# Performance work log

Measured on AMD Instinct MI355X. Metric: run time of the kernel, lower is better.

The kernel has to match this reference:

```python
import jax, jax.numpy as jnp
import numpy as np

N_NODES = 10000
N_EDGES = 640000
DIM = 128


def setup_inputs() -> dict:
    key = jax.random.key(0)
    ks = jax.random.split(key, 10)
    s = 1.0 / np.sqrt(DIM)
    return {
        "x": jax.random.normal(ks[0], (N_NODES, DIM), dtype=jnp.float32),
        "edge_index": jax.random.randint(ks[1], (2, N_EDGES), 0, N_NODES, dtype=jnp.int64),
        "fc_w": jax.random.normal(ks[2], (DIM, DIM), dtype=jnp.float32) * s,
        "fc_b": jax.random.normal(ks[3], (DIM,), dtype=jnp.float32) * s,
        "f_lw": jax.random.normal(ks[4], (DIM, DIM), dtype=jnp.float32) * s,
        "f_lb": jax.random.normal(ks[5], (DIM,), dtype=jnp.float32) * s,
        "f_rw": jax.random.normal(ks[6], (DIM, DIM), dtype=jnp.float32) * s,
        "n_lw": jax.random.normal(ks[7], (DIM, DIM), dtype=jnp.float32) * s,
        "n_lb": jax.random.normal(ks[8], (DIM,), dtype=jnp.float32) * s,
        "n_rw": jax.random.normal(ks[9], (DIM, DIM), dtype=jnp.float32) * s,
    }


def _sage_conv(h, src, dst, lw, lb, rw, n_nodes):
    # mean aggregation of source-node features at target nodes
    msg = h[src]                                                   # [E, D]
    summed = jax.ops.segment_sum(msg, dst, num_segments=n_nodes)   # [N, D]
    cnt = jax.ops.segment_sum(jnp.ones_like(dst, dtype=h.dtype), dst, num_segments=n_nodes)
    agg = summed / jnp.maximum(cnt, 1.0)[:, None]
    # PyG SAGEConv: lin_l(agg) + lin_r(x); lin_l has bias, lin_r does not
    return agg @ lw.T + lb + h @ rw.T


def reference(x, edge_index, fc_w, fc_b, f_lw, f_lb, f_rw, n_lw, n_lb, n_rw):
    n_nodes = x.shape[0]
    src, dst = edge_index[0], edge_index[1]
    inp = x @ fc_w.T + fc_b                                        # fc residual branch
    h = jax.nn.relu(_sage_conv(x, src, dst, f_lw, f_lb, f_rw, n_nodes))
    # dropout(p=0.3) is identity in eval mode
    h = _sage_conv(h, src, dst, n_lw, n_lb, n_rw, n_nodes)
    return jax.nn.relu(h + inp)
```

## Files before the change

### kernel.cpp

```cpp
#include <hip/hip_runtime.h>
#include <hip/hip_fp8.h>

#define NN 10000
#define NE 640000
#define DIM 128
#define NB2 625
#define RC2 1280
#define EPB 4096
#define G_FILL 157
#define MT1 157
#define NODECAP 128

typedef __attribute__((ext_vector_type(8))) short bf16x8;
typedef __attribute__((ext_vector_type(4))) float f32x4;

__device__ __forceinline__ unsigned short f2bf(float f) {
    unsigned u = __float_as_uint(f);
    u += 0x7FFFu + ((u >> 16) & 1u);
    return (unsigned short)(u >> 16);
}
__device__ __forceinline__ unsigned char f2f8(float f) {
    __hip_fp8_e4m3 t(f);
    return (unsigned char)t.__x;
}
__device__ __forceinline__ float f82f(unsigned char u) {
    __hip_fp8_e4m3 t;
    t.__x = (__hip_fp8_storage_t)u;
    return (float)t;
}
__device__ __forceinline__ bf16x8 cvt8(const float* p) {
    float4 v0 = *(const float4*)p;
    float4 v1 = *(const float4*)(p + 4);
    bf16x8 f;
    f[0] = (short)f2bf(v0.x); f[1] = (short)f2bf(v0.y);
    f[2] = (short)f2bf(v0.z); f[3] = (short)f2bf(v0.w);
    f[4] = (short)f2bf(v1.x); f[5] = (short)f2bf(v1.y);
    f[6] = (short)f2bf(v1.z); f[7] = (short)f2bf(v1.w);
    return f;
}

__device__ __forceinline__ void gather8(const unsigned char* __restrict__ g8,
                                        const unsigned short* lst,
                                        int deg, int d8, float* a) {
#pragma unroll
    for (int j = 0; j < 8; ++j) a[j] = 0.f;
    union U { uint2 v; unsigned char c[8]; };
    int r = 0;
    for (; r + 8 <= deg; r += 8) {
        U u[8];
#pragma unroll
        for (int t = 0; t < 8; ++t)
            u[t].v = *(const uint2*)(const void*)(g8 + (size_t)lst[r + t] * DIM + d8 * 8);
#pragma unroll
        for (int t = 0; t < 8; ++t)
#pragma unroll
            for (int j = 0; j < 8; ++j) a[j] += f82f(u[t].c[j]);
    }
    for (; r < deg; ++r) {
        U u0;
        u0.v = *(const uint2*)(const void*)(g8 + (size_t)lst[r] * DIM + d8 * 8);
#pragma unroll
        for (int j = 0; j < 8; ++j) a[j] += f82f(u0.c[j]);
    }
}

__global__ __launch_bounds__(256) void k1_k(
        const float* __restrict__ x,
        const int* __restrict__ src, const int* __restrict__ dst,
        const float* __restrict__ f_lw, const float* __restrict__ f_rw,
        const float* __restrict__ fc_w,
        unsigned char* __restrict__ xl8, float* __restrict__ xr, float* __restrict__ xc,
        int* __restrict__ gcur, unsigned* __restrict__ region) {
    __shared__ int start[NB2 + 1];
    __shared__ int cur[NB2];
    __shared__ int gbase[NB2];
    __shared__ int tsum[256];
    __shared__ unsigned sorted[EPB];
    const int b = blockIdx.x;
    const int tid = threadIdx.x;
    if (b < G_FILL) {
        for (int i = tid; i < NB2 + 1; i += 256) start[i] = 0;
        __syncthreads();
        int base = b * EPB;
        int nE = min(EPB, NE - base);
        unsigned pk[4][4];
        int kb[4][4];
        bool cv[4];
#pragma unroll
        for (int c = 0; c < 4; ++c) {
            int e = base + c * 1024 + tid * 4;
            cv[c] = (e < NE);
            if (cv[c]) {
                int4 s4 = *(const int4*)(src + e);
                int4 d4 = *(const int4*)(dst + e);
                pk[c][0] = ((unsigned)d4.x << 16) | (unsigned)s4.x;
                pk[c][1] = ((unsigned)d4.y << 16) | (unsigned)s4.y;
                pk[c][2] = ((unsigned)d4.z << 16) | (unsigned)s4.z;
                pk[c][3] = ((unsigned)d4.w << 16) | (unsigned)s4.w;
                kb[c][0] = d4.x >> 4; kb[c][1] = d4.y >> 4;
                kb[c][2] = d4.z >> 4; kb[c][3] = d4.w >> 4;
            }
        }
#pragma unroll
        for (int c = 0; c < 4; ++c)
            if (cv[c])
#pragma unroll
                for (int j = 0; j < 4; ++j) atomicAdd(&start[kb[c][j] + 1], 1);
        __syncthreads();
        {
            int s = 0;
            int i0 = 1 + tid * 3;
#pragma unroll
            for (int k = 0; k < 3; ++k) {
                int idx = i0 + k;
                if (idx < NB2 + 1) s += start[idx];
            }
            tsum[tid] = s;
            __syncthreads();
            for (int off = 1; off < 256; off <<= 1) {
                int v = 0;
                if (tid >= off) v = tsum[tid - off];
                __syncthreads();
                tsum[tid] += v;
                __syncthreads();
            }
            int run = (tid == 0) ? 0 : tsum[tid - 1];
#pragma unroll
            for (int k = 0; k < 3; ++k) {
                int idx = i0 + k;
                if (idx < NB2 + 1) { run += start[idx]; start[idx] = run; }
            }
        }
        __syncthreads();
        for (int i = tid; i < NB2; i += 256) cur[i] = start[i];
        __syncthreads();
#pragma unroll
        for (int c = 0; c < 4; ++c)
            if (cv[c])
#pragma unroll
                for (int j = 0; j < 4; ++j) {
                    int q = atomicAdd(&cur[kb[c][j]], 1);
                    sorted[q] = pk[c][j];
                }
        __syncthreads();
        for (int i = tid; i < NB2; i += 256) {
            int len = start[i + 1] - start[i];
            gbase[i] = (len > 0) ? atomicAdd(&gcur[i], len) : 0;
        }
        __syncthreads();
        for (int i = tid; i < nE; i += 256) {
            unsigned e = sorted[i];
            int bb = (int)(e >> 16) >> 4;
            int rel = gbase[bb] + (i - start[bb]);
            if (rel < RC2) region[(size_t)bb * RC2 + rel] = e;
        }
        return;
    }
    int jj = b - G_FILL;
    int plane = jj / MT1;
    int mt = jj - plane * MT1;
    const float* W = (plane == 0) ? f_lw : (plane == 1) ? f_rw : fc_w;
    int lane = tid & 63, wv = tid >> 6;
    int mr = lane & 15, q = lane >> 4;
    int m0 = mt * 64 + wv * 16;
    int mc = min(m0 + mr, NN - 1);
    bf16x8 afr[4];
#pragma unroll
    for (int kc = 0; kc < 4; ++kc)
        afr[kc] = cvt8(x + (size_t)mc * DIM + kc * 32 + q * 8);
    f32x4 acc[8];
#pragma unroll
    for (int nt = 0; nt < 8; ++nt) acc[nt] = (f32x4){0.f, 0.f, 0.f, 0.f};
#pragma unroll
    for (int nt = 0; nt < 8; ++nt) {
        const float* wp = W + (size_t)(nt * 16 + mr) * DIM;
#pragma unroll
        for (int kc = 0; kc < 4; ++kc) {
            bf16x8 wfr = cvt8(wp + kc * 32 + q * 8);
            acc[nt] = __builtin_amdgcn_mfma_f32_16x16x32_bf16(afr[kc], wfr, acc[nt], 0, 0, 0);
        }
    }
#pragma unroll
    for (int r = 0; r < 4; ++r) {
        int ms = m0 + q * 4 + r;
        if (ms >= NN) continue;
        if (plane == 0) {
#pragma unroll
            for (int nt = 0; nt < 8; ++nt)
                xl8[(size_t)ms * DIM + nt * 16 + mr] = f2f8(acc[nt][r]);
        } else {
            float* o = (plane == 1) ? xr : xc;
#pragma unroll
            for (int nt = 0; nt < 8; ++nt)
                o[(size_t)ms * DIM + nt * 16 + mr] = acc[nt][r];
        }
    }
}

__global__ __launch_bounds__(256) void k2_k(
        const unsigned char* __restrict__ xl8, const float* __restrict__ xr,
        const float* __restrict__ f_lb,
        const int* __restrict__ gcur, const unsigned* __restrict__ region,
        unsigned short* __restrict__ h1b, unsigned char* __restrict__ h18,
        unsigned short* __restrict__ glist, int* __restrict__ gcnt) {
    __shared__ int cnt[16];
    __shared__ unsigned short list[16][NODECAP];
    const int b = blockIdx.x;
    const int tid = threadIdx.x;
    if (tid < 16) cnt[tid] = 0;
    __syncthreads();
    const int n0 = b * 16;
    const int R = min(gcur[b], RC2);
    const unsigned* reg = region + (size_t)b * RC2;
    for (int i = tid; i < R; i += 256) {
        unsigned e = reg[i];
        int nl = (int)(e >> 16) - n0;
        if ((unsigned)nl < 16u) {
            int slot = atomicAdd(&cnt[nl], 1);
            if (slot < NODECAP) list[nl][slot] = (unsigned short)(e & 0xFFFFu);
        }
    }
    __syncthreads();
    {
        const int4* ls = (const int4*)&list[0][0];
        int4* gd = (int4*)(void*)(glist + (size_t)b * (16 * NODECAP));
        gd[tid] = ls[tid];
        if (tid < 16) gcnt[n0 + tid] = cnt[tid];
    }
    const int g = tid >> 4, d8 = tid & 15;
    const int node = n0 + g;
    const int trueDeg = cnt[g];
    const int deg = min(trueDeg, NODECAP);
    float a[8];
    gather8(xl8, &list[g][0], deg, d8, a);
    float inv = 1.f / fmaxf((float)trueDeg, 1.f);
    const float* xp = xr + (size_t)node * DIM + d8 * 8;
    float4 r0 = *(const float4*)xp;
    float4 r1 = *(const float4*)(xp + 4);
    const float* bp = f_lb + d8 * 8;
    float4 c0 = *(const float4*)bp;
    float4 c1 = *(const float4*)(bp + 4);
    float rv[8] = {r0.x, r0.y, r0.z, r0.w, r1.x, r1.y, r1.z, r1.w};
    float bv[8] = {c0.x, c0.y, c0.z, c0.w, c1.x, c1.y, c1.z, c1.w};
    union B { int4 v; unsigned short us[8]; } o;
    union U8 { uint2 v; unsigned char c[8]; } o8;
#pragma unroll
    for (int j = 0; j < 8; ++j) {
        float v = fmaxf(a[j] * inv + rv[j] + bv[j], 0.f);
        o.us[j] = f2bf(v);
        o8.c[j] = f2f8(v);
    }
    *(int4*)(void*)(h1b + (size_t)node * DIM + d8 * 8) = o.v;
    *(uint2*)(void*)(h18 + (size_t)node * DIM + d8 * 8) = o8.v;
}

__global__ __launch_bounds__(256) void k3_k(
        const unsigned char* __restrict__ h18, const unsigned short* __restrict__ h1b,
        const float* __restrict__ n_lw, const float* __restrict__ n_rw,
        const float* __restrict__ n_lb, const float* __restrict__ fc_b,
        const float* __restrict__ xc,
        const unsigned short* __restrict__ glist, const int* __restrict__ gcnt,
        float* __restrict__ out) {
    __shared__ int cnt[16];
    __shared__ unsigned short list[16][NODECAP];
    __shared__ unsigned short m1t[16][DIM];
    const int b = blockIdx.x;
    const int tid = threadIdx.x;
    {
        int4* ls = (int4*)&list[0][0];
        const int4* gs = (const int4*)(const void*)(glist + (size_t)b * (16 * NODECAP));
        ls[tid] = gs[tid];
        if (tid < 16) cnt[tid] = gcnt[b * 16 + tid];
    }
    __syncthreads();
    const int g = tid >> 4, d8 = tid & 15;
    const int trueDeg = cnt[g];
    const int deg = min(trueDeg, NODECAP);
    float a[8];
    gather8(h18, &list[g][0], deg, d8, a);
    float inv = 1.f / fmaxf((float)trueDeg, 1.f);
    union B { int4 v; unsigned short us[8]; } mo;
#pragma unroll
    for (int j = 0; j < 8; ++j) mo.us[j] = f2bf(a[j] * inv);
    *(int4*)(void*)(&m1t[g][d8 * 8]) = mo.v;
    __syncthreads();
    const int lane = tid & 63, wv = tid >> 6;
    const int mr = lane & 15, q = lane >> 4;
    const int m0 = b * 16;
    bf16x8 a0[4], a1[4];
#pragma unroll
    for (int kc = 0; kc < 4; ++kc) {
        a0[kc] = *(const bf16x8*)(const void*)(&m1t[mr][kc * 32 + q * 8]);
        a1[kc] = *(const bf16x8*)(const void*)(h1b + (size_t)(m0 + mr) * DIM + kc * 32 + q * 8);
    }
    f32x4 acc[2];
    acc[0] = (f32x4){0.f, 0.f, 0.f, 0.f};
    acc[1] = (f32x4){0.f, 0.f, 0.f, 0.f};
#pragma unroll
    for (int ntl = 0; ntl < 2; ++ntl) {
        int nt = wv * 2 + ntl;
        const float* w0p = n_lw + (size_t)(nt * 16 + mr) * DIM;
        const float* w1p = n_rw + (size_t)(nt * 16 + mr) * DIM;
#pragma unroll
        for (int kc = 0; kc < 4; ++kc) {
            bf16x8 wf0 = cvt8(w0p + kc * 32 + q * 8);
            acc[ntl] = __builtin_amdgcn_mfma_f32_16x16x32_bf16(a0[kc], wf0, acc[ntl], 0, 0, 0);
            bf16x8 wf1 = cvt8(w1p + kc * 32 + q * 8);
            acc[ntl] = __builtin_amdgcn_mfma_f32_16x16x32_bf16(a1[kc], wf1, acc[ntl], 0, 0, 0);
        }
    }
#pragma unroll
    for (int ntl = 0; ntl < 2; ++ntl) {
        int col = (wv * 2 + ntl) * 16 + mr;
        float bias = n_lb[col] + fc_b[col];
#pragma unroll
        for (int r = 0; r < 4; ++r) {
            int ms = m0 + q * 4 + r;
            float v = acc[ntl][r] + xc[(size_t)ms * DIM + col] + bias;
            out[(size_t)ms * DIM + col] = fmaxf(v, 0.f);
        }
    }
}

extern "C" void kernel_launch(void* const* d_in, const int* in_sizes, int n_in,
                              void* d_out, int out_size, void* d_ws, size_t ws_size,
                              hipStream_t stream) {
    const float* x    = (const float*)d_in[0];
    const int*   edge = (const int*)d_in[1];
    const float* fc_w = (const float*)d_in[2];
    const float* fc_b = (const float*)d_in[3];
    const float* f_lw = (const float*)d_in[4];
    const float* f_lb = (const float*)d_in[5];
    const float* f_rw = (const float*)d_in[6];
    const float* n_lw = (const float*)d_in[7];
    const float* n_lb = (const float*)d_in[8];
    const float* n_rw = (const float*)d_in[9];
    float* out = (float*)d_out;

    const int* src = edge;
    const int* dst = edge + NE;

    char* p = (char*)d_ws;
    float* xr = (float*)p;                    p += (size_t)NN * DIM * sizeof(float);
    float* xc = (float*)p;                    p += (size_t)NN * DIM * sizeof(float);
    unsigned short* h1b = (unsigned short*)p; p += (size_t)NN * DIM * sizeof(unsigned short);
    unsigned char* xl8 = (unsigned char*)p;   p += (size_t)NN * DIM;
    unsigned char* h18 = (unsigned char*)p;   p += (size_t)NN * DIM;
    unsigned short* glist = (unsigned short*)p; p += (size_t)NB2 * 16 * NODECAP * sizeof(unsigned short);
    int* gcnt = (int*)p;                      p += (size_t)NN * sizeof(int);
    int* gcur = (int*)p;                      p += 4096;
    unsigned* region = (unsigned*)p;

    hipMemsetAsync(gcur, 0, NB2 * sizeof(int), stream);
    k1_k<<<G_FILL + 3 * MT1, 256, 0, stream>>>(
        x, src, dst, f_lw, f_rw, fc_w, xl8, xr, xc, gcur, region);
    k2_k<<<NB2, 256, 0, stream>>>(xl8, xr, f_lb, gcur, region, h1b, h18, glist, gcnt);
    k3_k<<<NB2, 256, 0, stream>>>(h18, h1b, n_lw, n_rw, n_lb, fc_b, xc, glist, gcnt, out);
}
```

Before: 143.3 us.

## Fuse three kernels into one persistent kernel with grid barriers

Merges the bucket-fill/GEMM, first SAGE aggregation and second aggregation+GEMM kernels into a single launch of 628 blocks separated by software grid barriers on global atomics. Each block keeps its per-node edge list and its bf16 h1 tile in shared memory across phases, which removes the glist/gcnt/h1b global round-trips and two kernel launch gaps. It relies on all 628 blocks being co-resident (launch_bounds 256,3 on 256 CUs). If they are not, the spin barriers deadlock, and the barriers add spin/sleep latency.

```diff
diff --git a/kernel.cpp b/kernel.cpp
--- a/kernel.cpp
+++ b/kernel.cpp
@@ -10,6 +10,7 @@
 #define G_FILL 157
 #define MT1 157
 #define NODECAP 128
+#define GRID 628
 
 typedef __attribute__((ext_vector_type(8))) short bf16x8;
 typedef __attribute__((ext_vector_type(4))) float f32x4;
@@ -64,21 +65,39 @@
     }
 }
 
-__global__ __launch_bounds__(256) void k1_k(
+__device__ __forceinline__ void gridbar(int* bar) {
+    __syncthreads();
+    if (threadIdx.x == 0) {
+        __threadfence();
+        __hip_atomic_fetch_add(bar, 1, __ATOMIC_RELEASE, __HIP_MEMORY_SCOPE_AGENT);
+        while (__hip_atomic_load(bar, __ATOMIC_ACQUIRE, __HIP_MEMORY_SCOPE_AGENT) < GRID)
+            __builtin_amdgcn_s_sleep(8);
+        __threadfence();
+    }
+    __syncthreads();
+}
+
+__global__ __launch_bounds__(256, 3) void fused_k(
         const float* __restrict__ x,
         const int* __restrict__ src, const int* __restrict__ dst,
-        const float* __restrict__ f_lw, const float* __restrict__ f_rw,
-        const float* __restrict__ fc_w,
+        const float* __restrict__ f_lw, const float* __restrict__ f_lb,
+        const float* __restrict__ f_rw, const float* __restrict__ fc_w,
+        const float* __restrict__ fc_b, const float* __restrict__ n_lw,
+        const float* __restrict__ n_lb, const float* __restrict__ n_rw,
         unsigned char* __restrict__ xl8, float* __restrict__ xr, float* __restrict__ xc,
-        int* __restrict__ gcur, unsigned* __restrict__ region) {
-    __shared__ int start[NB2 + 1];
-    __shared__ int cur[NB2];
-    __shared__ int gbase[NB2];
-    __shared__ int tsum[256];
-    __shared__ unsigned sorted[EPB];
+        unsigned char* __restrict__ h18,
+        int* __restrict__ gcur, unsigned* __restrict__ region,
+        int* __restrict__ bar, float* __restrict__ out) {
+    __shared__ int sh[6228];
     const int b = blockIdx.x;
     const int tid = threadIdx.x;
+
     if (b < G_FILL) {
+        int* start = sh;
+        int* cur   = sh + 626;
+        int* gbase = sh + 1251;
+        int* tsum  = sh + 1876;
+        unsigned* sorted = (unsigned*)(sh + 2132);
         for (int i = tid; i < NB2 + 1; i += 256) start[i] = 0;
         __syncthreads();
         int base = b * EPB;
@@ -154,170 +173,144 @@
             int rel = gbase[bb] + (i - start[bb]);
             if (rel < RC2) region[(size_t)bb * RC2 + rel] = e;
         }
-        return;
-    }
-    int jj = b - G_FILL;
-    int plane = jj / MT1;
-    int mt = jj - plane * MT1;
-    const float* W = (plane == 0) ? f_lw : (plane == 1) ? f_rw : fc_w;
-    int lane = tid & 63, wv = tid >> 6;
-    int mr = lane & 15, q = lane >> 4;
-    int m0 = mt * 64 + wv * 16;
-    int mc = min(m0 + mr, NN - 1);
-    bf16x8 afr[4];
-#pragma unroll
-    for (int kc = 0; kc < 4; ++kc)
-        afr[kc] = cvt8(x + (size_t)mc * DIM + kc * 32 + q * 8);
-    f32x4 acc[8];
-#pragma unroll
-    for (int nt = 0; nt < 8; ++nt) acc[nt] = (f32x4){0.f, 0.f, 0.f, 0.f};
-#pragma unroll
-    for (int nt = 0; nt < 8; ++nt) {
-        const float* wp = W + (size_t)(nt * 16 + mr) * DIM;
-#pragma unroll
-        for (int kc = 0; kc < 4; ++kc) {
-            bf16x8 wfr = cvt8(wp + kc * 32 + q * 8);
-            acc[nt] = __builtin_amdgcn_mfma_f32_16x16x32_bf16(afr[kc], wfr, acc[nt], 0, 0, 0);
-        }
-    }
-#pragma unroll
-    for (int r = 0; r < 4; ++r) {
-        int ms = m0 + q * 4 + r;
-        if (ms >= NN) continue;
-        if (plane == 0) {
-#pragma unroll
-            for (int nt = 0; nt < 8; ++nt)
-                xl8[(size_t)ms * DIM + nt * 16 + mr] = f2f8(acc[nt][r]);
-        } else {
-            float* o = (plane == 1) ? xr : xc;
-#pragma unroll
-            for (int nt = 0; nt < 8; ++nt)
-                o[(size_t)ms * DIM + nt * 16 + mr] = acc[nt][r];
-        }
-    }
-}
-
-__global__ __launch_bounds__(256) void k2_k(
-        const unsigned char* __restrict__ xl8, const float* __restrict__ xr,
-        const float* __restrict__ f_lb,
-        const int* __restrict__ gcur, const unsigned* __restrict__ region,
-        unsigned short* __restrict__ h1b, unsigned char* __restrict__ h18,
-        unsigned short* __restrict__ glist, int* __restrict__ gcnt) {
-    __shared__ int cnt[16];
-    __shared__ unsigned short list[16][NODECAP];
-    const int b = blockIdx.x;
-    const int tid = threadIdx.x;
-    if (tid < 16) cnt[tid] = 0;
-    __syncthreads();
-    const int n0 = b * 16;
-    const int R = min(gcur[b], RC2);
-    const unsigned* reg = region + (size_t)b * RC2;
-    for (int i = tid; i < R; i += 256) {
-        unsigned e = reg[i];
-        int nl = (int)(e >> 16) - n0;
-        if ((unsigned)nl < 16u) {
-            int slot = atomicAdd(&cnt[nl], 1);
-            if (slot < NODECAP) list[nl][slot] = (unsigned short)(e & 0xFFFFu);
-        }
-    }
-    __syncthreads();
-    {
-        const int4* ls = (const int4*)&list[0][0];
-        int4* gd = (int4*)(void*)(glist + (size_t)b * (16 * NODECAP));
-        gd[tid] = ls[tid];
-        if (tid < 16) gcnt[n0 + tid] = cnt[tid];
-    }
-    const int g = tid >> 4, d8 = tid & 15;
-    const int node = n0 + g;
-    const int trueDeg = cnt[g];
-    const int deg = min(trueDeg, NODECAP);
-    float a[8];
-    gather8(xl8, &list[g][0], deg, d8, a);
-    float inv = 1.f / fmaxf((float)trueDeg, 1.f);
-    const float* xp = xr + (size_t)node * DIM + d8 * 8;
-    float4 r0 = *(const float4*)xp;
-    float4 r1 = *(const float4*)(xp + 4);
-    const float* bp = f_lb + d8 * 8;
-    float4 c0 = *(const float4*)bp;
-    float4 c1 = *(const float4*)(bp + 4);
-    float rv[8] = {r0.x, r0.y, r0.z, r0.w, r1.x, r1.y, r1.z, r1.w};
-    float bv[8] = {c0.x, c0.y, c0.z, c0.w, c1.x, c1.y, c1.z, c1.w};
-    union B { int4 v; unsigned short us[8]; } o;
-    union U8 { uint2 v; unsigned char c[8]; } o8;
-#pragma unroll
-    for (int j = 0; j < 8; ++j) {
-        float v = fmaxf(a[j] * inv + rv[j] + bv[j], 0.f);
-        o.us[j] = f2bf(v);
-        o8.c[j] = f2f8(v);
-    }
-    *(int4*)(void*)(h1b + (size_t)node * DIM + d8 * 8) = o.v;
-    *(uint2*)(void*)(h18 + (size_t)node * DIM + d8 * 8) = o8.v;
-}
-
-__global__ __launch_bounds__(256) void k3_k(
-        const unsigned char* __restrict__ h18, const unsigned short* __restrict__ h1b,
-        const float* __restrict__ n_lw, const float* __restrict__ n_rw,
-        const float* __restrict__ n_lb, const float* __restrict__ fc_b,
-        const float* __restrict__ xc,
-        const unsigned short* __restrict__ glist, const int* __restrict__ gcnt,
-        float* __restrict__ out) {
-    __shared__ int cnt[16];
-    __shared__ unsigned short list[16][NODECAP];
-    __shared__ unsigned short m1t[16][DIM];
-    const int b = blockIdx.x;
-    const int tid = threadIdx.x;
-    {
-        int4* ls = (int4*)&list[0][0];
-        const int4* gs = (const int4*)(const void*)(glist + (size_t)b * (16 * NODECAP));
-        ls[tid] = gs[tid];
-        if (tid < 16) cnt[tid] = gcnt[b * 16 + tid];
-    }
-    __syncthreads();
-    const int g = tid >> 4, d8 = tid & 15;
-    const int trueDeg = cnt[g];
-    const int deg = min(trueDeg, NODECAP);
-    float a[8];
-    gather8(h18, &list[g][0], deg, d8, a);
-    float inv = 1.f / fmaxf((float)trueDeg, 1.f);
-    union B { int4 v; unsigned short us[8]; } mo;
-#pragma unroll
-    for (int j = 0; j < 8; ++j) mo.us[j] = f2bf(a[j] * inv);
-    *(int4*)(void*)(&m1t[g][d8 * 8]) = mo.v;
-    __syncthreads();
-    const int lane = tid & 63, wv = tid >> 6;
-    const int mr = lane & 15, q = lane >> 4;
-    const int m0 = b * 16;
-    bf16x8 a0[4], a1[4];
-#pragma unroll
-    for (int kc = 0; kc < 4; ++kc) {
-        a0[kc] = *(const bf16x8*)(const void*)(&m1t[mr][kc * 32 + q * 8]);
-        a1[kc] = *(const bf16x8*)(const void*)(h1b + (size_t)(m0 + mr) * DIM + kc * 32 + q * 8);
-    }
-    f32x4 acc[2];
-    acc[0] = (f32x4){0.f, 0.f, 0.f, 0.f};
-    acc[1] = (f32x4){0.f, 0.f, 0.f, 0.f};
-#pragma unroll
-    for (int ntl = 0; ntl < 2; ++ntl) {
-        int nt = wv * 2 + ntl;
-        const float* w0p = n_lw + (size_t)(nt * 16 + mr) * DIM;
-        const float* w1p = n_rw + (size_t)(nt * 16 + mr) * DIM;
-#pragma unroll
-        for (int kc = 0; kc < 4; ++kc) {
-            bf16x8 wf0 = cvt8(w0p + kc * 32 + q * 8);
-            acc[ntl] = __builtin_amdgcn_mfma_f32_16x16x32_bf16(a0[kc], wf0, acc[ntl], 0, 0, 0);
-            bf16x8 wf1 = cvt8(w1p + kc * 32 + q * 8);
-            acc[ntl] = __builtin_amdgcn_mfma_f32_16x16x32_bf16(a1[kc], wf1, acc[ntl], 0, 0, 0);
-        }
-    }
-#pragma unroll
-    for (int ntl = 0; ntl < 2; ++ntl) {
-        int col = (wv * 2 + ntl) * 16 + mr;
-        float bias = n_lb[col] + fc_b[col];
+    } else {
+        int jj = b - G_FILL;
+        int plane = jj / MT1;
+        int mt = jj - plane * MT1;
+        const float* W = (plane == 0) ? f_lw : (plane == 1) ? f_rw : fc_w;
+        int lane = tid & 63, wv = tid >> 6;
+        int mr = lane & 15, q = lane >> 4;
+        int m0 = mt * 64 + wv * 16;
+        int mc = min(m0 + mr, NN - 1);
+        bf16x8 afr[4];
+#pragma unroll
+        for (int kc = 0; kc < 4; ++kc)
+            afr[kc] = cvt8(x + (size_t)mc * DIM + kc * 32 + q * 8);
+        f32x4 acc[8];
+#pragma unroll
+        for (int nt = 0; nt < 8; ++nt) acc[nt] = (f32x4){0.f, 0.f, 0.f, 0.f};
+#pragma unroll
+        for (int nt = 0; nt < 8; ++nt) {
+            const float* wp = W + (size_t)(nt * 16 + mr) * DIM;
+#pragma unroll
+            for (int kc = 0; kc < 4; ++kc) {
+                bf16x8 wfr = cvt8(wp + kc * 32 + q * 8);
+                acc[nt] = __builtin_amdgcn_mfma_f32_16x16x32_bf16(afr[kc], wfr, acc[nt], 0, 0, 0);
+            }
+        }
 #pragma unroll
         for (int r = 0; r < 4; ++r) {
             int ms = m0 + q * 4 + r;
-            float v = acc[ntl][r] + xc[(size_t)ms * DIM + col] + bias;
-            out[(size_t)ms * DIM + col] = fmaxf(v, 0.f);
+            if (ms < NN) {
+                if (plane == 0) {
+#pragma unroll
+                    for (int nt = 0; nt < 8; ++nt)
+                        xl8[(size_t)ms * DIM + nt * 16 + mr] = f2f8(acc[nt][r]);
+                } else {
+                    float* o = (plane == 1) ? xr : xc;
+#pragma unroll
+                    for (int nt = 0; nt < 8; ++nt)
+                        o[(size_t)ms * DIM + nt * 16 + mr] = acc[nt][r];
+                }
+            }
+        }
+    }
+    gridbar(&bar[0]);
+
+    int* cnt = sh;
+    unsigned short* list = (unsigned short*)(sh + 16);
+    unsigned short* h1t  = (unsigned short*)(sh + 1040);
+    unsigned short* m1t  = (unsigned short*)(sh + 2064);
+    const int g = tid >> 4, d8 = tid & 15;
+    if (b < NB2) {
+        if (tid < 16) cnt[tid] = 0;
+        __syncthreads();
+        const int n0 = b * 16;
+        const int R = min(gcur[b], RC2);
+        const unsigned* reg = region + (size_t)b * RC2;
+        for (int i = tid; i < R; i += 256) {
+            unsigned e = reg[i];
+            int nl = (int)(e >> 16) - n0;
+            if ((unsigned)nl < 16u) {
+                int slot = atomicAdd(&cnt[nl], 1);
+                if (slot < NODECAP) list[nl * NODECAP + slot] = (unsigned short)(e & 0xFFFFu);
+            }
+        }
+        __syncthreads();
+        const int node = n0 + g;
+        const int trueDeg = cnt[g];
+        const int deg = min(trueDeg, NODECAP);
+        float a[8];
+        gather8(xl8, list + g * NODECAP, deg, d8, a);
+        float inv = 1.f / fmaxf((float)trueDeg, 1.f);
+        const float* xp = xr + (size_t)node * DIM + d8 * 8;
+        float4 r0 = *(const float4*)xp;
+        float4 r1 = *(const float4*)(xp + 4);
+        const float* bp = f_lb + d8 * 8;
+        float4 c0 = *(const float4*)bp;
+        float4 c1 = *(const float4*)(bp + 4);
+        float rv[8] = {r0.x, r0.y, r0.z, r0.w, r1.x, r1.y, r1.z, r1.w};
+        float bv[8] = {c0.x, c0.y, c0.z, c0.w, c1.x, c1.y, c1.z, c1.w};
+        union B { int4 v; unsigned short us[8]; } o;
+        union U8 { uint2 v; unsigned char c[8]; } o8;
+#pragma unroll
+        for (int j = 0; j < 8; ++j) {
+            float v = fmaxf(a[j] * inv + rv[j] + bv[j], 0.f);
+            o.us[j] = f2bf(v);
+            o8.c[j] = f2f8(v);
+        }
+        *(int4*)(void*)(&h1t[g * DIM + d8 * 8]) = o.v;
+        *(uint2*)(void*)(h18 + (size_t)node * DIM + d8 * 8) = o8.v;
+    }
+    gridbar(&bar[1]);
+
+    if (b < NB2) {
+        const int trueDeg = cnt[g];
+        const int deg = min(trueDeg, NODECAP);
+        float a[8];
+        gather8(h18, list + g * NODECAP, deg, d8, a);
+        float inv = 1.f / fmaxf((float)trueDeg, 1.f);
+        union B { int4 v; unsigned short us[8]; } mo;
+#pragma unroll
+        for (int j = 0; j < 8; ++j) mo.us[j] = f2bf(a[j] * inv);
+        *(int4*)(void*)(&m1t[g * DIM + d8 * 8]) = mo.v;
+        __syncthreads();
+
+        const int lane = tid & 63, wv = tid >> 6;
+        const int mr = lane & 15, q = lane >> 4;
+        const int m0 = b * 16;
+        bf16x8 a0[4], a1[4];
+#pragma unroll
+        for (int kc = 0; kc < 4; ++kc) {
+            a0[kc] = *(const bf16x8*)(const void*)(&m1t[mr * DIM + kc * 32 + q * 8]);
+            a1[kc] = *(const bf16x8*)(const void*)(&h1t[mr * DIM + kc * 32 + q * 8]);
+        }
+        f32x4 acc[2];
+        acc[0] = (f32x4){0.f, 0.f, 0.f, 0.f};
+        acc[1] = (f32x4){0.f, 0.f, 0.f, 0.f};
+#pragma unroll
+        for (int ntl = 0; ntl < 2; ++ntl) {
+            int nt = wv * 2 + ntl;
+            const float* w0p = n_lw + (size_t)(nt * 16 + mr) * DIM;
+            const float* w1p = n_rw + (size_t)(nt * 16 + mr) * DIM;
+#pragma unroll
+            for (int kc = 0; kc < 4; ++kc) {
+                bf16x8 wf0 = cvt8(w0p + kc * 32 + q * 8);
+                acc[ntl] = __builtin_amdgcn_mfma_f32_16x16x32_bf16(a0[kc], wf0, acc[ntl], 0, 0, 0);
+                bf16x8 wf1 = cvt8(w1p + kc * 32 + q * 8);
+                acc[ntl] = __builtin_amdgcn_mfma_f32_16x16x32_bf16(a1[kc], wf1, acc[ntl], 0, 0, 0);
+            }
+        }
+#pragma unroll
+        for (int ntl = 0; ntl < 2; ++ntl) {
+            int col = (wv * 2 + ntl) * 16 + mr;
+            float bias = n_lb[col] + fc_b[col];
+#pragma unroll
+            for (int r = 0; r < 4; ++r) {
+                int ms = m0 + q * 4 + r;
+                float v = acc[ntl][r] + xc[(size_t)ms * DIM + col] + bias;
+                out[(size_t)ms * DIM + col] = fmaxf(v, 0.f);
+            }
         }
     }
 }
@@ -343,17 +336,14 @@
     char* p = (char*)d_ws;
     float* xr = (float*)p;                    p += (size_t)NN * DIM * sizeof(float);
     float* xc = (float*)p;                    p += (size_t)NN * DIM * sizeof(float);
-    unsigned short* h1b = (unsigned short*)p; p += (size_t)NN * DIM * sizeof(unsigned short);
     unsigned char* xl8 = (unsigned char*)p;   p += (size_t)NN * DIM;
     unsigned char* h18 = (unsigned char*)p;   p += (size_t)NN * DIM;
-    unsigned short* glist = (unsigned short*)p; p += (size_t)NB2 * 16 * NODECAP * sizeof(unsigned short);
-    int* gcnt = (int*)p;                      p += (size_t)NN * sizeof(int);
-    int* gcur = (int*)p;                      p += 4096;
+    int* gcur = (int*)p;
+    int* bar = gcur + 640;                    p += 4096;
     unsigned* region = (unsigned*)p;
 
-    hipMemsetAsync(gcur, 0, NB2 * sizeof(int), stream);
-    k1_k<<<G_FILL + 3 * MT1, 256, 0, stream>>>(
-        x, src, dst, f_lw, f_rw, fc_w, xl8, xr, xc, gcur, region);
-    k2_k<<<NB2, 256, 0, stream>>>(xl8, xr, f_lb, gcur, region, h1b, h18, glist, gcnt);
-    k3_k<<<NB2, 256, 0, stream>>>(h18, h1b, n_lw, n_rw, n_lb, fc_b, xc, glist, gcnt, out);
-}
+    hipMemsetAsync(gcur, 0, 4096, stream);
+    fused_k<<<GRID, 256, 0, stream>>>(
+        x, src, dst, f_lw, f_lb, f_rw, fc_w, fc_b, n_lw, n_lb, n_rw,
+        xl8, xr, xc, h18, gcur, region, bar, out);
+}
```

Result: slower. 375.4 us (+162.1%).

## Store xr/xc intermediates as bf16, widen gather unroll, hoist independent loads

Applied to the files above, without the earlier changes.

The xr and xc intermediate planes move from fp32 to bf16, halving their write traffic in k1 and read traffic in k2/k3. The edge gather loop now processes 16 neighbours per iteration instead of 8, giving more loads in flight. Loads that do not depend on the adjacency list (xr row, bias, h1b MFMA fragments) are hoisted ahead of the list-building and syncs so their latency overlaps. The cost is extra rounding error in the residual and fc branches and higher register use from the wider unroll.

```diff
diff --git a/kernel.cpp b/kernel.cpp
--- a/kernel.cpp
+++ b/kernel.cpp
@@ -19,6 +19,9 @@
     u += 0x7FFFu + ((u >> 16) & 1u);
     return (unsigned short)(u >> 16);
 }
+__device__ __forceinline__ float bf2f(unsigned short h) {
+    return __uint_as_float(((unsigned)h) << 16);
+}
 __device__ __forceinline__ unsigned char f2f8(float f) {
     __hip_fp8_e4m3 t(f);
     return (unsigned char)t.__x;
@@ -39,14 +42,24 @@
     return f;
 }
 
-__device__ __forceinline__ void gather8(const unsigned char* __restrict__ g8,
-                                        const unsigned short* lst,
-                                        int deg, int d8, float* a) {
+__device__ __forceinline__ void gather16(const unsigned char* __restrict__ g8,
+                                         const unsigned short* lst,
+                                         int deg, int d8, float* a) {
 #pragma unroll
     for (int j = 0; j < 8; ++j) a[j] = 0.f;
     union U { uint2 v; unsigned char c[8]; };
     int r = 0;
-    for (; r + 8 <= deg; r += 8) {
+    for (; r + 16 <= deg; r += 16) {
+        U u[16];
+#pragma unroll
+        for (int t = 0; t < 16; ++t)
+            u[t].v = *(const uint2*)(const void*)(g8 + (size_t)lst[r + t] * DIM + d8 * 8);
+#pragma unroll
+        for (int t = 0; t < 16; ++t)
+#pragma unroll
+            for (int j = 0; j < 8; ++j) a[j] += f82f(u[t].c[j]);
+    }
+    if (r + 8 <= deg) {
         U u[8];
 #pragma unroll
         for (int t = 0; t < 8; ++t)
@@ -55,6 +68,7 @@
         for (int t = 0; t < 8; ++t)
 #pragma unroll
             for (int j = 0; j < 8; ++j) a[j] += f82f(u[t].c[j]);
+        r += 8;
     }
     for (; r < deg; ++r) {
         U u0;
@@ -69,7 +83,8 @@
         const int* __restrict__ src, const int* __restrict__ dst,
         const float* __restrict__ f_lw, const float* __restrict__ f_rw,
         const float* __restrict__ fc_w,
-        unsigned char* __restrict__ xl8, float* __restrict__ xr, float* __restrict__ xc,
+        unsigned char* __restrict__ xl8, unsigned short* __restrict__ xr,
+        unsigned short* __restrict__ xc,
         int* __restrict__ gcur, unsigned* __restrict__ region) {
     __shared__ int start[NB2 + 1];
     __shared__ int cur[NB2];
@@ -189,16 +204,16 @@
             for (int nt = 0; nt < 8; ++nt)
                 xl8[(size_t)ms * DIM + nt * 16 + mr] = f2f8(acc[nt][r]);
         } else {
-            float* o = (plane == 1) ? xr : xc;
+            unsigned short* o = (plane == 1) ? xr : xc;
 #pragma unroll
             for (int nt = 0; nt < 8; ++nt)
-                o[(size_t)ms * DIM + nt * 16 + mr] = acc[nt][r];
+                o[(size_t)ms * DIM + nt * 16 + mr] = f2bf(acc[nt][r]);
         }
     }
 }
 
 __global__ __launch_bounds__(256) void k2_k(
-        const unsigned char* __restrict__ xl8, const float* __restrict__ xr,
+        const unsigned char* __restrict__ xl8, const unsigned short* __restrict__ xr,
         const float* __restrict__ f_lb,
         const int* __restrict__ gcur, const unsigned* __restrict__ region,
         unsigned short* __restrict__ h1b, unsigned char* __restrict__ h18,
@@ -207,9 +222,15 @@
     __shared__ unsigned short list[16][NODECAP];
     const int b = blockIdx.x;
     const int tid = threadIdx.x;
+    const int g = tid >> 4, d8 = tid & 15;
+    const int n0 = b * 16;
+    const int node = n0 + g;
+    bf16x8 rv8 = *(const bf16x8*)(const void*)(xr + (size_t)node * DIM + d8 * 8);
+    const float* bp = f_lb + d8 * 8;
+    float4 c0 = *(const float4*)bp;
+    float4 c1 = *(const float4*)(bp + 4);
     if (tid < 16) cnt[tid] = 0;
     __syncthreads();
-    const int n0 = b * 16;
     const int R = min(gcur[b], RC2);
     const unsigned* reg = region + (size_t)b * RC2;
     for (int i = tid; i < R; i += 256) {
@@ -227,26 +248,17 @@
         gd[tid] = ls[tid];
         if (tid < 16) gcnt[n0 + tid] = cnt[tid];
     }
-    const int g = tid >> 4, d8 = tid & 15;
-    const int node = n0 + g;
     const int trueDeg = cnt[g];
     const int deg = min(trueDeg, NODECAP);
     float a[8];
-    gather8(xl8, &list[g][0], deg, d8, a);
+    gather16(xl8, &list[g][0], deg, d8, a);
     float inv = 1.f / fmaxf((float)trueDeg, 1.f);
-    const float* xp = xr + (size_t)node * DIM + d8 * 8;
-    float4 r0 = *(const float4*)xp;
-    float4 r1 = *(const float4*)(xp + 4);
-    const float* bp = f_lb + d8 * 8;
-    float4 c0 = *(const float4*)bp;
-    float4 c1 = *(const float4*)(bp + 4);
-    float rv[8] = {r0.x, r0.y, r0.z, r0.w, r1.x, r1.y, r1.z, r1.w};
     float bv[8] = {c0.x, c0.y, c0.z, c0.w, c1.x, c1.y, c1.z, c1.w};
     union B { int4 v; unsigned short us[8]; } o;
     union U8 { uint2 v; unsigned char c[8]; } o8;
 #pragma unroll
     for (int j = 0; j < 8; ++j) {
-        float v = fmaxf(a[j] * inv + rv[j] + bv[j], 0.f);
+        float v = fmaxf(a[j] * inv + bf2f((unsigned short)rv8[j]) + bv[j], 0.f);
         o.us[j] = f2bf(v);
         o8.c[j] = f2f8(v);
     }
@@ -258,7 +270,7 @@
         const unsigned char* __restrict__ h18, const unsigned short* __restrict__ h1b,
         const float* __restrict__ n_lw, const float* __restrict__ n_rw,
         const float* __restrict__ n_lb, const float* __restrict__ fc_b,
-        const float* __restrict__ xc,
+        const unsigned short* __restrict__ xc,
         const unsigned short* __restrict__ glist, const int* __restrict__ gcnt,
         float* __restrict__ out) {
     __shared__ int cnt[16];
@@ -266,6 +278,13 @@
     __shared__ unsigned short m1t[16][DIM];
     const int b = blockIdx.x;
     const int tid = threadIdx.x;
+    const int lane = tid & 63, wv = tid >> 6;
+    const int mr = lane & 15, q = lane >> 4;
+    const int m0 = b * 16;
+    bf16x8 a1[4];
+#pragma unroll
+    for (int kc = 0; kc < 4; ++kc)
+        a1[kc] = *(const bf16x8*)(const void*)(h1b + (size_t)(m0 + mr) * DIM + kc * 32 + q * 8);
     {
         int4* ls = (int4*)&list[0][0];
         const int4* gs = (const int4*)(const void*)(glist + (size_t)b * (16 * NODECAP));
@@ -277,22 +296,17 @@
     const int trueDeg = cnt[g];
     const int deg = min(trueDeg, NODECAP);
     float a[8];
-    gather8(h18, &list[g][0], deg, d8, a);
+    gather16(h18, &list[g][0], deg, d8, a);
     float inv = 1.f / fmaxf((float)trueDeg, 1.f);
     union B { int4 v; unsigned short us[8]; } mo;
 #pragma unroll
     for (int j = 0; j < 8; ++j) mo.us[j] = f2bf(a[j] * inv);
     *(int4*)(void*)(&m1t[g][d8 * 8]) = mo.v;
     __syncthreads();
-    const int lane = tid & 63, wv = tid >> 6;
-    const int mr = lane & 15, q = lane >> 4;
-    const int m0 = b * 16;
-    bf16x8 a0[4], a1[4];
-#pragma unroll
-    for (int kc = 0; kc < 4; ++kc) {
+    bf16x8 a0[4];
+#pragma unroll
+    for (int kc = 0; kc < 4; ++kc)
         a0[kc] = *(const bf16x8*)(const void*)(&m1t[mr][kc * 32 + q * 8]);
-        a1[kc] = *(const bf16x8*)(const void*)(h1b + (size_t)(m0 + mr) * DIM + kc * 32 + q * 8);
-    }
     f32x4 acc[2];
     acc[0] = (f32x4){0.f, 0.f, 0.f, 0.f};
     acc[1] = (f32x4){0.f, 0.f, 0.f, 0.f};
@@ -316,7 +330,7 @@
 #pragma unroll
         for (int r = 0; r < 4; ++r) {
             int ms = m0 + q * 4 + r;
-            float v = acc[ntl][r] + xc[(size_t)ms * DIM + col] + bias;
+            float v = acc[ntl][r] + bf2f(xc[(size_t)ms * DIM + col]) + bias;
             out[(size_t)ms * DIM + col] = fmaxf(v, 0.f);
         }
     }
@@ -341,8 +355,8 @@
     const int* dst = edge + NE;
 
     char* p = (char*)d_ws;
-    float* xr = (float*)p;                    p += (size_t)NN * DIM * sizeof(float);
-    float* xc = (float*)p;                    p += (size_t)NN * DIM * sizeof(float);
+    unsigned short* xr = (unsigned short*)p;  p += (size_t)NN * DIM * sizeof(unsigned short);
+    unsigned short* xc = (unsigned short*)p;  p += (size_t)NN * DIM * sizeof(unsigned short);
     unsigned short* h1b = (unsigned short*)p; p += (size_t)NN * DIM * sizeof(unsigned short);
     unsigned char* xl8 = (unsigned char*)p;   p += (size_t)NN * DIM;
     unsigned char* h18 = (unsigned char*)p;   p += (size_t)NN * DIM;
```

New measurement: 144.3 us. Within noise of the previous version (+0.7%).
